# Kernel optimization log

Hardware: AMD Instinct MI355X
Metric: run time of the kernel (lower is better)

## Reference

```python
import jax, jax.numpy as jnp
import numpy as np

MARGIN = 0.2


def setup_inputs() -> dict:
    key = jax.random.key(0)
    ks = jax.random.split(key, 6)
    B, E = 8192, 1024
    return {
        "A_is_t": jax.random.normal(ks[0], (B, E), dtype=jnp.float32),
        "A_em_t": jax.random.normal(ks[1], (B, E), dtype=jnp.float32),
        "m": jax.random.normal(ks[2], (B, E), dtype=jnp.float32),
        "tr_m": jax.random.normal(ks[3], (B, E), dtype=jnp.float32),
        "W": jax.random.normal(ks[4], (E, E), dtype=jnp.float32) * (1.0 / np.sqrt(E)),
        "b": jax.random.normal(ks[5], (E,), dtype=jnp.float32) * 0.01,
    }


def reference(A_is_t, A_em_t, m, tr_m, W, b):
    # Linear layer: w(A) = A @ W.T + b  (torch nn.Linear convention)
    wA_is = A_is_t @ W.T + b  # [B, E]
    wA_em = A_em_t @ W.T + b  # [B, E]
    # Original builds full [B,B] score matrices but only uses the diagonal;
    # diagonal entries are exactly rowwise dots, computed directly here.
    d_is = jnp.einsum("be,be->b", m, wA_is)
    d_em = jnp.einsum("be,be->b", m, wA_em)
    d_is_trm = jnp.einsum("be,be->b", tr_m, wA_is)
    d_em_trm = jnp.einsum("be,be->b", tr_m, wA_em)
    diag_is_all = 0.4 * d_is + 0.6 * d_is_trm  # [B]
    diag_em_all = 0.6 * d_em_trm + 0.4 * d_em  # [B]
    cost_s = jnp.maximum(MARGIN + diag_is_all - diag_em_all, 0.0)  # hinge
    return cost_s.reshape(-1, 1).sum(axis=0)  # [1], matches cost_s.sum(0)
```

## Files before the change

### kernel.cpp

```cpp
#include <hip/hip_runtime.h>
#include <hip/hip_bf16.h>

#define B_ROWS 8192
#define E_DIM  1024
#define MARGIN 0.2f

#define BM 128
#define BN 128
#define BK 32
#define NSTEPS (E_DIM / BK)

typedef __bf16 bf16x8 __attribute__((ext_vector_type(8)));
typedef float  f32x4  __attribute__((ext_vector_type(4)));

__device__ __forceinline__ void gload_lds16(const void* g, void* l) {
    __builtin_amdgcn_global_load_lds(
        (__attribute__((address_space(1))) void*)(g),
        (__attribute__((address_space(3))) void*)(l),
        16, 0, 0);
}

#define GATE4() do { asm volatile("s_waitcnt vmcnt(4)" ::: "memory"); \
                     __builtin_amdgcn_sched_barrier(0); } while (0)
#define GATE0() do { asm volatile("s_waitcnt vmcnt(0)" ::: "memory"); \
                     __builtin_amdgcn_sched_barrier(0); } while (0)
#define RBAR()  do { __builtin_amdgcn_s_barrier(); \
                     __builtin_amdgcn_sched_barrier(0); } while (0)
#define LGKM0() do { asm volatile("s_waitcnt lgkmcnt(0)" ::: "memory"); \
                     __builtin_amdgcn_sched_barrier(0); } while (0)

__global__ __launch_bounds__(256)
void prep_combo(const float* __restrict__ m, const float* __restrict__ trm,
                __bf16* __restrict__ c,
                const float* __restrict__ W, __bf16* __restrict__ Wt) {
    __shared__ float tile[32][33];
    if (blockIdx.x < 4096) {
        size_t i = ((size_t)blockIdx.x * blockDim.x + threadIdx.x) * 8;
        float4 m0 = *(const float4*)(m + i);
        float4 m1 = *(const float4*)(m + i + 4);
        float4 t0 = *(const float4*)(trm + i);
        float4 t1 = *(const float4*)(trm + i + 4);
        bf16x8 v;
        v[0] = (__bf16)(0.4f*m0.x + 0.6f*t0.x);
        v[1] = (__bf16)(0.4f*m0.y + 0.6f*t0.y);
        v[2] = (__bf16)(0.4f*m0.z + 0.6f*t0.z);
        v[3] = (__bf16)(0.4f*m0.w + 0.6f*t0.w);
        v[4] = (__bf16)(0.4f*m1.x + 0.6f*t1.x);
        v[5] = (__bf16)(0.4f*m1.y + 0.6f*t1.y);
        v[6] = (__bf16)(0.4f*m1.z + 0.6f*t1.z);
        v[7] = (__bf16)(0.4f*m1.w + 0.6f*t1.w);
        *(bf16x8*)(c + i) = v;
    } else {
        const int tb = blockIdx.x - 4096;
        const int bx = (tb & 31) * 32;
        const int by = (tb >> 5) * 32;
        const int tx = threadIdx.x & 31;
        const int ty0 = threadIdx.x >> 5;
#pragma unroll
        for (int r = 0; r < 32; r += 8)
            tile[r + ty0][tx] = W[(size_t)(by + r + ty0) * E_DIM + bx + tx];
        __syncthreads();
#pragma unroll
        for (int r = 0; r < 32; r += 8)
            Wt[(size_t)(bx + r + ty0) * E_DIM + by + tx] = (__bf16)tile[tx][r + ty0];
    }
}

__global__ __launch_bounds__(256)
void gemm_dot(const __bf16* __restrict__ Cm, const __bf16* __restrict__ Wt,
              const float* __restrict__ Ais, const float* __restrict__ Aem,
              float* __restrict__ delta) {
    __shared__ __bf16 As[3][BM * BK];
    __shared__ __bf16 Bs[3][BN * BK];

    const int tid  = threadIdx.x;
    const int lane = tid & 63;
    const int wave = tid >> 6;
    const int lr   = lane & 15;
    const int hi   = lane >> 4;
    const int wr   = wave >> 1, wc = wave & 1;

    const int bid  = blockIdx.x;
    const int xcd  = bid & 7;
    const int q    = bid >> 3;
    const int rb   = (xcd * 8 + (q >> 3)) * BM;
    const int cb   = (q & 7) * BN;

    auto stage = [&](int slot, int k0) {
#pragma unroll
        for (int i = 0; i < 2; ++i) {
            int off = i * 4096 + tid * 16;
            int row = off >> 6;
            int kb  = off & 63;
            gload_lds16((const char*)Cm + ((size_t)(rb + row) * E_DIM + k0) * 2 + kb,
                        (char*)(&As[slot][0]) + off);
            gload_lds16((const char*)Wt + ((size_t)(cb + row) * E_DIM + k0) * 2 + kb,
                        (char*)(&Bs[slot][0]) + off);
        }
    };

    f32x4 acc[4][4] = {};

    stage(0, 0);
    stage(1, BK);

    int s0 = 0, s1 = 1, s2 = 2;
    for (int t = 0; t < NSTEPS; ++t) {
        if (t + 1 < NSTEPS) GATE4(); else GATE0();
        RBAR();

        bf16x8 a[4], b[4];
#pragma unroll
        for (int mi = 0; mi < 4; ++mi)
            a[mi] = *(const bf16x8*)(&As[s0][(wr * 64 + mi * 16 + lr) * BK + hi * 8]);
#pragma unroll
        for (int ni = 0; ni < 4; ++ni)
            b[ni] = *(const bf16x8*)(&Bs[s0][(wc * 64 + ni * 16 + lr) * BK + hi * 8]);
        LGKM0();

        if (t + 2 < NSTEPS) stage(s2, (t + 2) * BK);

        __builtin_amdgcn_s_setprio(1);
#pragma unroll
        for (int mi = 0; mi < 4; ++mi)
#pragma unroll
            for (int ni = 0; ni < 4; ++ni)
                acc[mi][ni] = __builtin_amdgcn_mfma_f32_16x16x32_bf16(
                    a[mi], b[ni], acc[mi][ni], 0, 0, 0);
        __builtin_amdgcn_s_setprio(0);

        int tmp = s0; s0 = s1; s1 = s2; s2 = tmp;
    }

    const int colbase = cb + wc * 64 + lr;
    const int rowbase = rb + wr * 64 + hi * 4;
#pragma unroll
    for (int mi = 0; mi < 4; ++mi) {
#pragma unroll
        for (int jj = 0; jj < 4; ++jj) {
            const int r = rowbase + mi * 16 + jj;
            float v = 0.f;
#pragma unroll
            for (int ni = 0; ni < 4; ++ni) {
                const size_t idx = (size_t)r * E_DIM + colbase + ni * 16;
                v += acc[mi][ni][jj] * (Ais[idx] - Aem[idx]);
            }
            v += __shfl_xor(v, 1);
            v += __shfl_xor(v, 2);
            v += __shfl_xor(v, 4);
            v += __shfl_xor(v, 8);
            if (lr == 0) atomicAdd(&delta[r], v);
        }
    }
}

__global__ void hinge_sum(const float* __restrict__ delta, float* __restrict__ out) {
    float s = 0.f;
    for (int i = threadIdx.x; i < B_ROWS; i += 256)
        s += fmaxf(MARGIN + delta[i], 0.f);
#pragma unroll
    for (int off = 32; off > 0; off >>= 1) s += __shfl_down(s, off);
    __shared__ float wsum[4];
    int lane = threadIdx.x & 63, w = threadIdx.x >> 6;
    if (lane == 0) wsum[w] = s;
    __syncthreads();
    if (threadIdx.x == 0) out[0] = wsum[0] + wsum[1] + wsum[2] + wsum[3];
}

extern "C" void kernel_launch(void* const* d_in, const int* in_sizes, int n_in,
                              void* d_out, int out_size, void* d_ws, size_t ws_size,
                              hipStream_t stream) {
    const float* A_is = (const float*)d_in[0];
    const float* A_em = (const float*)d_in[1];
    const float* m    = (const float*)d_in[2];
    const float* tr_m = (const float*)d_in[3];
    const float* W    = (const float*)d_in[4];
    float* out = (float*)d_out;

    char* ws = (char*)d_ws;
    __bf16* c     = (__bf16*)ws;
    __bf16* wt    = (__bf16*)(ws + (size_t)16 * 1024 * 1024);
    float*  delta = (float*) (ws + (size_t)18 * 1024 * 1024);

    hipMemsetAsync(delta, 0, B_ROWS * sizeof(float), stream);
    prep_combo<<<5120, 256, 0, stream>>>(m, tr_m, c, W, wt);
    gemm_dot<<<512, 256, 0, stream>>>(c, wt, A_is, A_em, delta);
    hinge_sum<<<1, 256, 0, stream>>>(delta, out);
}
```

Measured before the change: 61.23 us.

## Load GEMM operands directly to registers and fold delta zeroing into prep

The GEMM drops the LDS triple-buffer staging with barriers and instead has each wave load its bf16 fragments straight from global memory into registers, double-buffered and fully unrolled. The separate memset of the delta accumulator is replaced by extra blocks in the prep kernel, which removes one launch. The trade-off is that without LDS sharing each fragment is fetched by several waves, so global/L2 traffic rises, and register pressure goes up.

```diff
diff --git a/kernel.cpp b/kernel.cpp
--- a/kernel.cpp
+++ b/kernel.cpp
@@ -4,36 +4,17 @@
 #define B_ROWS 8192
 #define E_DIM  1024
 #define MARGIN 0.2f
-
-#define BM 128
-#define BN 128
 #define BK 32
 #define NSTEPS (E_DIM / BK)
 
 typedef __bf16 bf16x8 __attribute__((ext_vector_type(8)));
 typedef float  f32x4  __attribute__((ext_vector_type(4)));
 
-__device__ __forceinline__ void gload_lds16(const void* g, void* l) {
-    __builtin_amdgcn_global_load_lds(
-        (__attribute__((address_space(1))) void*)(g),
-        (__attribute__((address_space(3))) void*)(l),
-        16, 0, 0);
-}
-
-#define GATE4() do { asm volatile("s_waitcnt vmcnt(4)" ::: "memory"); \
-                     __builtin_amdgcn_sched_barrier(0); } while (0)
-#define GATE0() do { asm volatile("s_waitcnt vmcnt(0)" ::: "memory"); \
-                     __builtin_amdgcn_sched_barrier(0); } while (0)
-#define RBAR()  do { __builtin_amdgcn_s_barrier(); \
-                     __builtin_amdgcn_sched_barrier(0); } while (0)
-#define LGKM0() do { asm volatile("s_waitcnt lgkmcnt(0)" ::: "memory"); \
-                     __builtin_amdgcn_sched_barrier(0); } while (0)
-
 __global__ __launch_bounds__(256)
 void prep_combo(const float* __restrict__ m, const float* __restrict__ trm,
                 __bf16* __restrict__ c,
-                const float* __restrict__ W, __bf16* __restrict__ Wt) {
-    __shared__ float tile[32][33];
+                const float* __restrict__ W, __bf16* __restrict__ Wt,
+                float* __restrict__ delta) {
     if (blockIdx.x < 4096) {
         size_t i = ((size_t)blockIdx.x * blockDim.x + threadIdx.x) * 8;
         float4 m0 = *(const float4*)(m + i);
@@ -50,7 +31,8 @@
         v[6] = (__bf16)(0.4f*m1.z + 0.6f*t1.z);
         v[7] = (__bf16)(0.4f*m1.w + 0.6f*t1.w);
         *(bf16x8*)(c + i) = v;
-    } else {
+    } else if (blockIdx.x < 5120) {
+        __shared__ float tile[32][33];
         const int tb = blockIdx.x - 4096;
         const int bx = (tb & 31) * 32;
         const int by = (tb >> 5) * 32;
@@ -63,6 +45,8 @@
 #pragma unroll
         for (int r = 0; r < 32; r += 8)
             Wt[(size_t)(bx + r + ty0) * E_DIM + by + tx] = (__bf16)tile[tx][r + ty0];
+    } else {
+        delta[(blockIdx.x - 5120) * 256 + threadIdx.x] = 0.f;
     }
 }
 
@@ -70,9 +54,6 @@
 void gemm_dot(const __bf16* __restrict__ Cm, const __bf16* __restrict__ Wt,
               const float* __restrict__ Ais, const float* __restrict__ Aem,
               float* __restrict__ delta) {
-    __shared__ __bf16 As[3][BM * BK];
-    __shared__ __bf16 Bs[3][BN * BK];
-
     const int tid  = threadIdx.x;
     const int lane = tid & 63;
     const int wave = tid >> 6;
@@ -80,56 +61,41 @@
     const int hi   = lane >> 4;
     const int wr   = wave >> 1, wc = wave & 1;
 
-    const int bid  = blockIdx.x;
-    const int xcd  = bid & 7;
-    const int q    = bid >> 3;
-    const int rb   = (xcd * 8 + (q >> 3)) * BM;
-    const int cb   = (q & 7) * BN;
+    const int bid = blockIdx.x;
+    const int xcd = bid & 7;
+    const int q   = bid >> 3;
+    const int rb  = (xcd * 8 + (q >> 3)) * 128;
+    const int cb  = (q & 7) * 128;
 
-    auto stage = [&](int slot, int k0) {
+    const __bf16* pa = Cm + (size_t)(rb + wr * 64 + lr) * E_DIM + hi * 8;
+    const __bf16* pb = Wt + (size_t)(cb + wc * 64 + lr) * E_DIM + hi * 8;
+
+    bf16x8 a0[4], b0[4], a1[4], b1[4];
+    f32x4 acc[4][4] = {};
+
+    auto loads = [&](bf16x8* A, bf16x8* B, int k) {
 #pragma unroll
-        for (int i = 0; i < 2; ++i) {
-            int off = i * 4096 + tid * 16;
-            int row = off >> 6;
-            int kb  = off & 63;
-            gload_lds16((const char*)Cm + ((size_t)(rb + row) * E_DIM + k0) * 2 + kb,
-                        (char*)(&As[slot][0]) + off);
-            gload_lds16((const char*)Wt + ((size_t)(cb + row) * E_DIM + k0) * 2 + kb,
-                        (char*)(&Bs[slot][0]) + off);
+        for (int i = 0; i < 4; ++i) {
+            A[i] = *(const bf16x8*)(pa + (size_t)(i * 16) * E_DIM + k);
+            B[i] = *(const bf16x8*)(pb + (size_t)(i * 16) * E_DIM + k);
         }
     };
-
-    f32x4 acc[4][4] = {};
-
-    stage(0, 0);
-    stage(1, BK);
-
-    int s0 = 0, s1 = 1, s2 = 2;
-    for (int t = 0; t < NSTEPS; ++t) {
-        if (t + 1 < NSTEPS) GATE4(); else GATE0();
-        RBAR();
-
-        bf16x8 a[4], b[4];
-#pragma unroll
-        for (int mi = 0; mi < 4; ++mi)
-            a[mi] = *(const bf16x8*)(&As[s0][(wr * 64 + mi * 16 + lr) * BK + hi * 8]);
-#pragma unroll
-        for (int ni = 0; ni < 4; ++ni)
-            b[ni] = *(const bf16x8*)(&Bs[s0][(wc * 64 + ni * 16 + lr) * BK + hi * 8]);
-        LGKM0();
-
-        if (t + 2 < NSTEPS) stage(s2, (t + 2) * BK);
-
-        __builtin_amdgcn_s_setprio(1);
+    auto mfmas = [&](bf16x8* A, bf16x8* B) {
 #pragma unroll
         for (int mi = 0; mi < 4; ++mi)
 #pragma unroll
             for (int ni = 0; ni < 4; ++ni)
                 acc[mi][ni] = __builtin_amdgcn_mfma_f32_16x16x32_bf16(
-                    a[mi], b[ni], acc[mi][ni], 0, 0, 0);
-        __builtin_amdgcn_s_setprio(0);
+                    A[mi], B[ni], acc[mi][ni], 0, 0, 0);
+    };
 
-        int tmp = s0; s0 = s1; s1 = s2; s2 = tmp;
+    loads(a0, b0, 0);
+#pragma unroll
+    for (int t = 0; t < NSTEPS; t += 2) {
+        loads(a1, b1, (t + 1) * BK);
+        mfmas(a0, b0);
+        if (t + 2 < NSTEPS) loads(a0, b0, (t + 2) * BK);
+        mfmas(a1, b1);
     }
 
     const int colbase = cb + wc * 64 + lr;
@@ -182,8 +148,7 @@
     __bf16* wt    = (__bf16*)(ws + (size_t)16 * 1024 * 1024);
     float*  delta = (float*) (ws + (size_t)18 * 1024 * 1024);
 
-    hipMemsetAsync(delta, 0, B_ROWS * sizeof(float), stream);
-    prep_combo<<<5120, 256, 0, stream>>>(m, tr_m, c, W, wt);
+    prep_combo<<<5152, 256, 0, stream>>>(m, tr_m, c, W, wt, delta);
     gemm_dot<<<512, 256, 0, stream>>>(c, wt, A_is, A_em, delta);
     hinge_sum<<<1, 256, 0, stream>>>(delta, out);
 }
```

After: 95.77 us. 56.4% more time.

## Switch GEMM operands to FP8 e4m3 with swizzled LDS and fused delta zeroing

Applied to the files above, without the earlier changes.

Quantizes the combined m/tr_m matrix and the transposed weight to FP8 e4m3 (weight pre-scaled by 16) and uses fp8 MFMA instructions with BK=64, halving operand bytes in global memory and LDS. LDS reads use an XOR swizzle to avoid bank conflicts. The delta memset is folded into the prep kernel as extra blocks, removing a separate launch. FP8 quantization adds significant rounding error to the dot products, which may exceed tolerance for the hinge sum.

```diff
diff --git a/kernel.cpp b/kernel.cpp
--- a/kernel.cpp
+++ b/kernel.cpp
@@ -1,17 +1,15 @@
 #include <hip/hip_runtime.h>
 #include <hip/hip_bf16.h>
+#include <hip/hip_fp8.h>
 
 #define B_ROWS 8192
 #define E_DIM  1024
 #define MARGIN 0.2f
-
-#define BM 128
-#define BN 128
-#define BK 32
+#define BK 64
 #define NSTEPS (E_DIM / BK)
-
-typedef __bf16 bf16x8 __attribute__((ext_vector_type(8)));
-typedef float  f32x4  __attribute__((ext_vector_type(4)));
+#define WSCALE 16.0f
+
+typedef float f32x4 __attribute__((ext_vector_type(4)));
 
 __device__ __forceinline__ void gload_lds16(const void* g, void* l) {
     __builtin_amdgcn_global_load_lds(
@@ -29,28 +27,33 @@
 #define LGKM0() do { asm volatile("s_waitcnt lgkmcnt(0)" ::: "memory"); \
                      __builtin_amdgcn_sched_barrier(0); } while (0)
 
+__device__ __forceinline__ unsigned char to_fp8(float x) {
+    return __hip_fp8_e4m3(x).__x;
+}
+
 __global__ __launch_bounds__(256)
 void prep_combo(const float* __restrict__ m, const float* __restrict__ trm,
-                __bf16* __restrict__ c,
-                const float* __restrict__ W, __bf16* __restrict__ Wt) {
-    __shared__ float tile[32][33];
+                unsigned char* __restrict__ c8,
+                const float* __restrict__ W, unsigned char* __restrict__ Wt8,
+                float* __restrict__ delta) {
     if (blockIdx.x < 4096) {
         size_t i = ((size_t)blockIdx.x * blockDim.x + threadIdx.x) * 8;
         float4 m0 = *(const float4*)(m + i);
         float4 m1 = *(const float4*)(m + i + 4);
         float4 t0 = *(const float4*)(trm + i);
         float4 t1 = *(const float4*)(trm + i + 4);
-        bf16x8 v;
-        v[0] = (__bf16)(0.4f*m0.x + 0.6f*t0.x);
-        v[1] = (__bf16)(0.4f*m0.y + 0.6f*t0.y);
-        v[2] = (__bf16)(0.4f*m0.z + 0.6f*t0.z);
-        v[3] = (__bf16)(0.4f*m0.w + 0.6f*t0.w);
-        v[4] = (__bf16)(0.4f*m1.x + 0.6f*t1.x);
-        v[5] = (__bf16)(0.4f*m1.y + 0.6f*t1.y);
-        v[6] = (__bf16)(0.4f*m1.z + 0.6f*t1.z);
-        v[7] = (__bf16)(0.4f*m1.w + 0.6f*t1.w);
-        *(bf16x8*)(c + i) = v;
-    } else {
+        union { unsigned char b[8]; unsigned long long u; } r;
+        r.b[0] = to_fp8(0.4f*m0.x + 0.6f*t0.x);
+        r.b[1] = to_fp8(0.4f*m0.y + 0.6f*t0.y);
+        r.b[2] = to_fp8(0.4f*m0.z + 0.6f*t0.z);
+        r.b[3] = to_fp8(0.4f*m0.w + 0.6f*t0.w);
+        r.b[4] = to_fp8(0.4f*m1.x + 0.6f*t1.x);
+        r.b[5] = to_fp8(0.4f*m1.y + 0.6f*t1.y);
+        r.b[6] = to_fp8(0.4f*m1.z + 0.6f*t1.z);
+        r.b[7] = to_fp8(0.4f*m1.w + 0.6f*t1.w);
+        *(unsigned long long*)(c8 + i) = r.u;
+    } else if (blockIdx.x < 5120) {
+        __shared__ float tile[32][33];
         const int tb = blockIdx.x - 4096;
         const int bx = (tb & 31) * 32;
         const int by = (tb >> 5) * 32;
@@ -62,16 +65,18 @@
         __syncthreads();
 #pragma unroll
         for (int r = 0; r < 32; r += 8)
-            Wt[(size_t)(bx + r + ty0) * E_DIM + by + tx] = (__bf16)tile[tx][r + ty0];
+            Wt8[(size_t)(bx + r + ty0) * E_DIM + by + tx] =
+                to_fp8(tile[tx][r + ty0] * WSCALE);
+    } else {
+        delta[(blockIdx.x - 5120) * 256 + threadIdx.x] = 0.f;
     }
 }
 
 __global__ __launch_bounds__(256)
-void gemm_dot(const __bf16* __restrict__ Cm, const __bf16* __restrict__ Wt,
+void gemm_dot(const unsigned char* __restrict__ Cm, const unsigned char* __restrict__ Wt,
               const float* __restrict__ Ais, const float* __restrict__ Aem,
               float* __restrict__ delta) {
-    __shared__ __bf16 As[3][BM * BK];
-    __shared__ __bf16 Bs[3][BN * BK];
+    __shared__ char smem[49152];
 
     const int tid  = threadIdx.x;
     const int lane = tid & 63;
@@ -80,22 +85,22 @@
     const int hi   = lane >> 4;
     const int wr   = wave >> 1, wc = wave & 1;
 
-    const int bid  = blockIdx.x;
-    const int xcd  = bid & 7;
-    const int q    = bid >> 3;
-    const int rb   = (xcd * 8 + (q >> 3)) * BM;
-    const int cb   = (q & 7) * BN;
+    const int bid = blockIdx.x;
+    const int xcd = bid & 7;
+    const int q   = bid >> 3;
+    const int rb  = (xcd * 8 + (q >> 3)) * 128;
+    const int cb  = (q & 7) * 128;
 
     auto stage = [&](int slot, int k0) {
 #pragma unroll
         for (int i = 0; i < 2; ++i) {
-            int off = i * 4096 + tid * 16;
-            int row = off >> 6;
-            int kb  = off & 63;
-            gload_lds16((const char*)Cm + ((size_t)(rb + row) * E_DIM + k0) * 2 + kb,
-                        (char*)(&As[slot][0]) + off);
-            gload_lds16((const char*)Wt + ((size_t)(cb + row) * E_DIM + k0) * 2 + kb,
-                        (char*)(&Bs[slot][0]) + off);
+            const int off = i * 4096 + tid * 16;
+            const int row = off >> 6;
+            const int kb  = (off & 63) ^ ((row & 7) << 3);
+            gload_lds16(Cm + (size_t)(rb + row) * E_DIM + k0 + kb,
+                        smem + slot * 8192 + off);
+            gload_lds16(Wt + (size_t)(cb + row) * E_DIM + k0 + kb,
+                        smem + 24576 + slot * 8192 + off);
         }
     };
 
@@ -109,24 +114,38 @@
         if (t + 1 < NSTEPS) GATE4(); else GATE0();
         RBAR();
 
-        bf16x8 a[4], b[4];
+        const char* Ab = smem + s0 * 8192;
+        const char* Bb = smem + 24576 + s0 * 8192;
+        const int swz = (lr & 7) << 3;
+        const int o0  = (hi * 8) ^ swz;
+        const int o1  = (32 + hi * 8) ^ swz;
+        long a0[4], a1[4], b0[4], b1[4];
+#pragma unroll
+        for (int mi = 0; mi < 4; ++mi) {
+            const int ro = (wr * 64 + mi * 16 + lr) * 64;
+            a0[mi] = *(const long*)(Ab + ro + o0);
+            a1[mi] = *(const long*)(Ab + ro + o1);
+        }
+#pragma unroll
+        for (int ni = 0; ni < 4; ++ni) {
+            const int ro = (wc * 64 + ni * 16 + lr) * 64;
+            b0[ni] = *(const long*)(Bb + ro + o0);
+            b1[ni] = *(const long*)(Bb + ro + o1);
+        }
+        LGKM0();
+
+        if (t + 2 < NSTEPS) stage(s2, (t + 2) * BK);
+
+        __builtin_amdgcn_s_setprio(1);
 #pragma unroll
         for (int mi = 0; mi < 4; ++mi)
-            a[mi] = *(const bf16x8*)(&As[s0][(wr * 64 + mi * 16 + lr) * BK + hi * 8]);
-#pragma unroll
-        for (int ni = 0; ni < 4; ++ni)
-            b[ni] = *(const bf16x8*)(&Bs[s0][(wc * 64 + ni * 16 + lr) * BK + hi * 8]);
-        LGKM0();
-
-        if (t + 2 < NSTEPS) stage(s2, (t + 2) * BK);
-
-        __builtin_amdgcn_s_setprio(1);
-#pragma unroll
-        for (int mi = 0; mi < 4; ++mi)
-#pragma unroll
-            for (int ni = 0; ni < 4; ++ni)
-                acc[mi][ni] = __builtin_amdgcn_mfma_f32_16x16x32_bf16(
-                    a[mi], b[ni], acc[mi][ni], 0, 0, 0);
+#pragma unroll
+            for (int ni = 0; ni < 4; ++ni) {
+                acc[mi][ni] = __builtin_amdgcn_mfma_f32_16x16x32_fp8_fp8(
+                    a0[mi], b0[ni], acc[mi][ni], 0, 0, 0);
+                acc[mi][ni] = __builtin_amdgcn_mfma_f32_16x16x32_fp8_fp8(
+                    a1[mi], b1[ni], acc[mi][ni], 0, 0, 0);
+            }
         __builtin_amdgcn_s_setprio(0);
 
         int tmp = s0; s0 = s1; s1 = s2; s2 = tmp;
@@ -149,7 +168,7 @@
             v += __shfl_xor(v, 2);
             v += __shfl_xor(v, 4);
             v += __shfl_xor(v, 8);
-            if (lr == 0) atomicAdd(&delta[r], v);
+            if (lr == 0) atomicAdd(&delta[r], v * (1.0f / WSCALE));
         }
     }
 }
@@ -178,12 +197,11 @@
     float* out = (float*)d_out;
 
     char* ws = (char*)d_ws;
-    __bf16* c     = (__bf16*)ws;
-    __bf16* wt    = (__bf16*)(ws + (size_t)16 * 1024 * 1024);
-    float*  delta = (float*) (ws + (size_t)18 * 1024 * 1024);
-
-    hipMemsetAsync(delta, 0, B_ROWS * sizeof(float), stream);
-    prep_combo<<<5120, 256, 0, stream>>>(m, tr_m, c, W, wt);
-    gemm_dot<<<512, 256, 0, stream>>>(c, wt, A_is, A_em, delta);
+    unsigned char* c8  = (unsigned char*)ws;
+    unsigned char* wt8 = (unsigned char*)(ws + (size_t)8 * 1024 * 1024);
+    float*         delta = (float*)(ws + (size_t)9 * 1024 * 1024);
+
+    prep_combo<<<5152, 256, 0, stream>>>(m, tr_m, c8, W, wt8, delta);
+    gemm_dot<<<512, 256, 0, stream>>>(c8, wt8, A_is, A_em, delta);
     hinge_sum<<<1, 256, 0, stream>>>(delta, out);
 }
```

New measurement: 49.56 us. -19.1%, faster.
